# Kernel optimization log

Hardware: AMD Instinct MI355X
Metric: run time of the kernel (lower is better)

## Reference

```python
import jax, jax.numpy as jnp
import numpy as np
from jax import lax

N_INPUTS = 8
N_OUTPUTS = 4
N_RESERVOIR = 2048
T = 4096
SPECTRAL_RADIUS = 0.95
NOISE = 0.001


def setup_inputs() -> dict:
    key = jax.random.key(0)
    ks = jax.random.split(key, 8)
    inputs = jax.random.normal(ks[0], (T, N_INPUTS), dtype=jnp.float32)
    outputs = jax.random.normal(ks[1], (T, N_OUTPUTS), dtype=jnp.float32)
    # recurrent weights: uniform(-0.5, 0.5), rescaled to spectral radius ~0.95.
    # For a uniform(-0.5,0.5) NxN matrix the spectral radius is ~ sqrt(N/12)
    # (circular law), used here in place of an explicit eigendecomposition.
    w_raw = jax.random.uniform(ks[2], (N_RESERVOIR, N_RESERVOIR), dtype=jnp.float32) - 0.5
    radius = jnp.sqrt(N_RESERVOIR / 12.0)
    w = w_raw * (SPECTRAL_RADIUS / radius)
    w_in = jax.random.uniform(ks[3], (N_RESERVOIR, N_INPUTS), dtype=jnp.float32) * 2.0 - 1.0
    w_feedb = jax.random.uniform(ks[4], (N_RESERVOIR, N_OUTPUTS), dtype=jnp.float32) * 2.0 - 1.0
    # readout (nn.Linear): weight [n_out, R+n_in], bias [n_out]
    fan_in = N_RESERVOIR + N_INPUTS
    bound = 1.0 / np.sqrt(fan_in)
    lin_w = jax.random.uniform(ks[5], (N_OUTPUTS, fan_in), dtype=jnp.float32, minval=-bound, maxval=bound)
    lin_b = jax.random.uniform(ks[6], (N_OUTPUTS,), dtype=jnp.float32, minval=-bound, maxval=bound)
    # per-step regularization noise: noise * (uniform - 0.5), pre-drawn for determinism
    noise_seq = NOISE * (jax.random.uniform(ks[7], (T, N_RESERVOIR), dtype=jnp.float32) - 0.5)
    return {"inputs": inputs, "outputs": outputs, "w": w, "w_in": w_in,
            "w_feedb": w_feedb, "lin_w": lin_w, "lin_b": lin_b, "noise_seq": noise_seq}


def reference(inputs, outputs, w, w_in, w_feedb, lin_w, lin_b, noise_seq):
    # Echo-state recurrence: x_n = tanh(w @ x_{n-1} + w_in @ u_n + w_feedb @ y_{n-1}) + noise_n
    # States row 0 stays zero (original loop starts at n=1).
    R = w.shape[0]

    def step(x, per_step):
        u_n, y_prev, nz = per_step
        x_new = jnp.tanh(w @ x + w_in @ u_n + w_feedb @ y_prev) + nz
        return x_new, x_new

    x0 = jnp.zeros((R,), dtype=inputs.dtype)
    _, xs = lax.scan(step, x0, (inputs[1:], outputs[:-1], noise_seq[1:]))  # [T-1, R]

    zero_row_x = jnp.zeros((1, R), dtype=inputs.dtype)
    zero_row_u = jnp.zeros((1, inputs.shape[1]), dtype=inputs.dtype)
    states_x = jnp.concatenate([zero_row_x, xs], axis=0)              # [T, R]
    states_u = jnp.concatenate([zero_row_u, inputs[1:]], axis=0)       # [T, n_in]
    states = jnp.concatenate([states_x, states_u], axis=1)             # [T, R+n_in]

    out = states @ lin_w.T + lin_b                                     # [T, n_out]
    return out
```

## Files before the change

kernel.cpp:

```cpp
#include <hip/hip_runtime.h>

#define T_STEPS 4096
#define RSIZE   2048
#define N_IN    8
#define N_OUT   4
#define NWG     256
#define NT      256
#define LIN_STRIDE  (RSIZE + N_IN)
#define SENTINEL    0x7FC00000u

typedef float v4 __attribute__((ext_vector_type(4)));


__global__ __launch_bounds__(256) void init_kernel(v4* __restrict__ states4) {
    int idx = blockIdx.x * 256 + threadIdx.x;
    const float s = __uint_as_float(SENTINEL);
    v4 v = (idx < RSIZE / 4) ? (v4){0.f, 0.f, 0.f, 0.f} : (v4){s, s, s, s};
    states4[idx] = v;
}

__device__ __forceinline__ float dot4(v4 a, v4 b) {
    float s = a.x * b.x;
    s = fmaf(a.y, b.y, s);
    s = fmaf(a.z, b.z, s);
    s = fmaf(a.w, b.w, s);
    return s;
}

__global__ __launch_bounds__(NT, 1) void reservoir_kernel(
    const float* __restrict__ W,
    const float* __restrict__ Win,
    const float* __restrict__ Wfb,
    const float* __restrict__ inputs,
    const float* __restrict__ outputs,
    const float* __restrict__ noise,
    float* __restrict__ states)
{
    const int g    = blockIdx.x;
    const int t    = threadIdx.x;
    const int lane = t & 63;
    const int wv   = t >> 6;
    const int wid  = g * 4 + wv;
    const int r0   = wid * 2;

    v4 wreg[2][8];
    #pragma unroll
    for (int i = 0; i < 2; ++i)
        #pragma unroll
        for (int c = 0; c < 8; ++c)
            wreg[i][c] = *(const v4*)(W + (size_t)(r0 + i) * RSIZE + c * 256 + lane * 4);

    float win[N_IN] = {0}, wfb[N_OUT] = {0};
    if (lane < 2) {
        const int r = r0 + lane;
        #pragma unroll
        for (int j = 0; j < N_IN; ++j)  win[j] = Win[r * N_IN + j];
        #pragma unroll
        for (int k = 0; k < N_OUT; ++k) wfb[k] = Wfb[r * N_OUT + k];
    }

    __shared__ v4 xsh[2][RSIZE / 4];
    const int fi0 = wv * 128 + lane;
    const int fi1 = wv * 128 + 64 + lane;

    float cur_pre = 0.0f, cur_nz = 0.0f;
    if (lane < 2) {
        const int r = r0 + lane;
        cur_nz = noise[(size_t)RSIZE + r];
        v4 i0 = *(const v4*)(inputs + N_IN);
        v4 i1 = *(const v4*)(inputs + N_IN + 4);
        v4 o0 = *(const v4*)(outputs);
        float p = 0.0f;
        p = fmaf(win[0], i0.x, p); p = fmaf(win[1], i0.y, p);
        p = fmaf(win[2], i0.z, p); p = fmaf(win[3], i0.w, p);
        p = fmaf(win[4], i1.x, p); p = fmaf(win[5], i1.y, p);
        p = fmaf(win[6], i1.z, p); p = fmaf(win[7], i1.w, p);
        p = fmaf(wfb[0], o0.x, p); p = fmaf(wfb[1], o0.y, p);
        p = fmaf(wfb[2], o0.z, p); p = fmaf(wfb[3], o0.w, p);
        cur_pre = p;
    }

    for (int n = 1; n < T_STEPS; ++n) {
        const bool hn = (n + 1 < T_STEPS);
        v4 ni0 = {0.f,0.f,0.f,0.f}, ni1 = {0.f,0.f,0.f,0.f}, no0 = {0.f,0.f,0.f,0.f};
        float nnz = 0.0f;
        if (lane < 2 && hn) {
            ni0 = *(const v4*)(inputs + (size_t)(n + 1) * N_IN);
            ni1 = *(const v4*)(inputs + (size_t)(n + 1) * N_IN + 4);
            no0 = *(const v4*)(outputs + (size_t)n * N_OUT);
            nnz = noise[(size_t)(n + 1) * RSIZE + r0 + lane];
        }

        const volatile v4* base =
            (const volatile v4*)(states + (size_t)(n - 1) * RSIZE);
        v4 a = {0.f, 0.f, 0.f, 0.f}, b = {0.f, 0.f, 0.f, 0.f};
        bool done = false;
        for (;;) {
            if (!done) {
                a = base[fi0];
                b = base[fi1];
                done = (__float_as_uint(a.x) != SENTINEL) &
                       (__float_as_uint(a.y) != SENTINEL) &
                       (__float_as_uint(a.z) != SENTINEL) &
                       (__float_as_uint(a.w) != SENTINEL) &
                       (__float_as_uint(b.x) != SENTINEL) &
                       (__float_as_uint(b.y) != SENTINEL) &
                       (__float_as_uint(b.z) != SENTINEL) &
                       (__float_as_uint(b.w) != SENTINEL);
            }
            if (__all(done)) break;
            __builtin_amdgcn_s_sleep(1);
        }

        const int p = (n - 1) & 1;
        xsh[p][fi0] = a;
        xsh[p][fi1] = b;
        __syncthreads();

        float a0 = 0.f, a1 = 0.f, b0 = 0.f, b1 = 0.f;
        #pragma unroll
        for (int c = 0; c < 4; ++c) {
            v4 x0 = xsh[p][c * 64 + lane];
            v4 x1 = xsh[p][(c + 4) * 64 + lane];
            a0 += dot4(wreg[0][c], x0);
            b0 += dot4(wreg[0][c + 4], x1);
            a1 += dot4(wreg[1][c], x0);
            b1 += dot4(wreg[1][c + 4], x1);
        }
        float acc0 = a0 + b0;
        float acc1 = a1 + b1;

        float mine  = (lane & 1) ? acc1 : acc0;
        float other = (lane & 1) ? acc0 : acc1;
        mine += __shfl_xor(other, 1, 64);
        mine += __shfl_xor(mine, 2, 64);
        mine += __shfl_xor(mine, 4, 64);
        mine += __shfl_xor(mine, 8, 64);
        mine += __shfl_xor(mine, 16, 64);
        mine += __shfl_xor(mine, 32, 64);

        if (lane < 2) {
            float xn = tanhf(mine + cur_pre) + cur_nz;
            *(volatile float*)(states + (size_t)n * RSIZE + r0 + lane) = xn;
        }

        if (lane < 2 && hn) {
            float pnext = 0.0f;
            pnext = fmaf(win[0], ni0.x, pnext); pnext = fmaf(win[1], ni0.y, pnext);
            pnext = fmaf(win[2], ni0.z, pnext); pnext = fmaf(win[3], ni0.w, pnext);
            pnext = fmaf(win[4], ni1.x, pnext); pnext = fmaf(win[5], ni1.y, pnext);
            pnext = fmaf(win[6], ni1.z, pnext); pnext = fmaf(win[7], ni1.w, pnext);
            pnext = fmaf(wfb[0], no0.x, pnext); pnext = fmaf(wfb[1], no0.y, pnext);
            pnext = fmaf(wfb[2], no0.z, pnext); pnext = fmaf(wfb[3], no0.w, pnext);
            cur_pre = pnext;
            cur_nz  = nnz;
        }
    }
}

__global__ __launch_bounds__(256) void readout_kernel(
    const float* __restrict__ states,
    const float* __restrict__ inputs,
    const float* __restrict__ lin_w,
    const float* __restrict__ lin_b,
    float* __restrict__ out)
{
    const int ti   = blockIdx.x;
    const int tid  = threadIdx.x;
    const int lane = tid & 63;
    const int wave = tid >> 6;
    const int c0   = tid * 8;

    const float* xp = states + (size_t)ti * RSIZE + c0;
    v4 xa = *(const v4*)xp;
    v4 xb = *(const v4*)(xp + 4);

    float acc[N_OUT];
    #pragma unroll
    for (int o = 0; o < N_OUT; ++o) {
        const float* lp = lin_w + (size_t)o * LIN_STRIDE + c0;
        v4 la = *(const v4*)lp;
        v4 lb = *(const v4*)(lp + 4);
        acc[o] = dot4(la, xa) + dot4(lb, xb);
    }

    #pragma unroll
    for (int m = 1; m < 64; m <<= 1) {
        #pragma unroll
        for (int o = 0; o < N_OUT; ++o) acc[o] += __shfl_xor(acc[o], m, 64);
    }

    __shared__ float red[4][N_OUT];
    if (lane == 0) {
        #pragma unroll
        for (int o = 0; o < N_OUT; ++o) red[wave][o] = acc[o];
    }
    __syncthreads();

    if (tid < N_OUT) {
        float s = red[0][tid] + red[1][tid] + red[2][tid] + red[3][tid] + lin_b[tid];
        if (ti > 0) {
            #pragma unroll
            for (int j = 0; j < N_IN; ++j)
                s = fmaf(lin_w[(size_t)tid * LIN_STRIDE + RSIZE + j],
                         inputs[ti * N_IN + j], s);
        }
        out[ti * N_OUT + tid] = s;
    }
}

extern "C" void kernel_launch(void* const* d_in, const int* in_sizes, int n_in,
                              void* d_out, int out_size, void* d_ws, size_t ws_size,
                              hipStream_t stream) {
    const float* inputs  = (const float*)d_in[0];
    const float* outputs = (const float*)d_in[1];
    const float* W       = (const float*)d_in[2];
    const float* Win     = (const float*)d_in[3];
    const float* Wfb     = (const float*)d_in[4];
    const float* lin_w   = (const float*)d_in[5];
    const float* lin_b   = (const float*)d_in[6];
    const float* noise   = (const float*)d_in[7];
    float* out = (float*)d_out;

    float* states = (float*)d_ws;

    hipLaunchKernelGGL(init_kernel, dim3((T_STEPS * RSIZE / 4) / 256), dim3(256), 0,
                       stream, (v4*)states);
    hipLaunchKernelGGL(reservoir_kernel, dim3(NWG), dim3(NT), 0, stream,
                       W, Win, Wfb, inputs, outputs, noise, states);
    hipLaunchKernelGGL(readout_kernel, dim3(T_STEPS), dim3(256), 0, stream,
                       states, inputs, lin_w, lin_b, out);
}
```

Before: 8.104 ms.

## Have each wave poll full state vector directly, dropping LDS staging and block barrier

Each wave now reads the whole previous state vector from global memory and polls every element for the sentinel itself. This removes the shared-memory staging copy and the __syncthreads that coupled the four waves of a workgroup. The cost is four times as many global/L2 loads per step, with each wave spinning on all 2048 entries. Per-step input loads are made volatile and an explicit waitcnt is added after the state store.

```diff
diff --git a/kernel.cpp b/kernel.cpp
--- a/kernel.cpp
+++ b/kernel.cpp
@@ -25,6 +25,13 @@
     s = fmaf(a.z, b.z, s);
     s = fmaf(a.w, b.w, s);
     return s;
+}
+
+__device__ __forceinline__ bool ok4(v4 a) {
+    return (__float_as_uint(a.x) != SENTINEL) &
+           (__float_as_uint(a.y) != SENTINEL) &
+           (__float_as_uint(a.z) != SENTINEL) &
+           (__float_as_uint(a.w) != SENTINEL);
 }
 
 __global__ __launch_bounds__(NT, 1) void reservoir_kernel(
@@ -59,10 +66,6 @@
         for (int k = 0; k < N_OUT; ++k) wfb[k] = Wfb[r * N_OUT + k];
     }
 
-    __shared__ v4 xsh[2][RSIZE / 4];
-    const int fi0 = wv * 128 + lane;
-    const int fi1 = wv * 128 + 64 + lane;
-
     float cur_pre = 0.0f, cur_nz = 0.0f;
     if (lane < 2) {
         const int r = r0 + lane;
@@ -85,48 +88,42 @@
         v4 ni0 = {0.f,0.f,0.f,0.f}, ni1 = {0.f,0.f,0.f,0.f}, no0 = {0.f,0.f,0.f,0.f};
         float nnz = 0.0f;
         if (lane < 2 && hn) {
-            ni0 = *(const v4*)(inputs + (size_t)(n + 1) * N_IN);
-            ni1 = *(const v4*)(inputs + (size_t)(n + 1) * N_IN + 4);
-            no0 = *(const v4*)(outputs + (size_t)n * N_OUT);
-            nnz = noise[(size_t)(n + 1) * RSIZE + r0 + lane];
+            ni0 = *(const volatile v4*)(inputs + (size_t)(n + 1) * N_IN);
+            ni1 = *(const volatile v4*)(inputs + (size_t)(n + 1) * N_IN + 4);
+            no0 = *(const volatile v4*)(outputs + (size_t)n * N_OUT);
+            nnz = *(const volatile float*)(noise + (size_t)(n + 1) * RSIZE + r0 + lane);
         }
 
         const volatile v4* base =
             (const volatile v4*)(states + (size_t)(n - 1) * RSIZE);
-        v4 a = {0.f, 0.f, 0.f, 0.f}, b = {0.f, 0.f, 0.f, 0.f};
+        v4 x0, x1, x2, x3, x4, x5, x6, x7;
         bool done = false;
         for (;;) {
             if (!done) {
-                a = base[fi0];
-                b = base[fi1];
-                done = (__float_as_uint(a.x) != SENTINEL) &
-                       (__float_as_uint(a.y) != SENTINEL) &
-                       (__float_as_uint(a.z) != SENTINEL) &
-                       (__float_as_uint(a.w) != SENTINEL) &
-                       (__float_as_uint(b.x) != SENTINEL) &
-                       (__float_as_uint(b.y) != SENTINEL) &
-                       (__float_as_uint(b.z) != SENTINEL) &
-                       (__float_as_uint(b.w) != SENTINEL);
+                x0 = base[0 * 64 + lane];
+                x1 = base[1 * 64 + lane];
+                x2 = base[2 * 64 + lane];
+                x3 = base[3 * 64 + lane];
+                x4 = base[4 * 64 + lane];
+                x5 = base[5 * 64 + lane];
+                x6 = base[6 * 64 + lane];
+                x7 = base[7 * 64 + lane];
+                done = ok4(x0) & ok4(x1) & ok4(x2) & ok4(x3) &
+                       ok4(x4) & ok4(x5) & ok4(x6) & ok4(x7);
             }
             if (__all(done)) break;
             __builtin_amdgcn_s_sleep(1);
         }
 
-        const int p = (n - 1) & 1;
-        xsh[p][fi0] = a;
-        xsh[p][fi1] = b;
-        __syncthreads();
-
-        float a0 = 0.f, a1 = 0.f, b0 = 0.f, b1 = 0.f;
-        #pragma unroll
-        for (int c = 0; c < 4; ++c) {
-            v4 x0 = xsh[p][c * 64 + lane];
-            v4 x1 = xsh[p][(c + 4) * 64 + lane];
-            a0 += dot4(wreg[0][c], x0);
-            b0 += dot4(wreg[0][c + 4], x1);
-            a1 += dot4(wreg[1][c], x0);
-            b1 += dot4(wreg[1][c + 4], x1);
-        }
+        float a0, a1, b0, b1;
+        a0  = dot4(wreg[0][0], x0); a1  = dot4(wreg[1][0], x0);
+        b0  = dot4(wreg[0][4], x4); b1  = dot4(wreg[1][4], x4);
+        a0 += dot4(wreg[0][1], x1); a1 += dot4(wreg[1][1], x1);
+        b0 += dot4(wreg[0][5], x5); b1 += dot4(wreg[1][5], x5);
+        a0 += dot4(wreg[0][2], x2); a1 += dot4(wreg[1][2], x2);
+        b0 += dot4(wreg[0][6], x6); b1 += dot4(wreg[1][6], x6);
+        a0 += dot4(wreg[0][3], x3); a1 += dot4(wreg[1][3], x3);
+        b0 += dot4(wreg[0][7], x7); b1 += dot4(wreg[1][7], x7);
         float acc0 = a0 + b0;
         float acc1 = a1 + b1;
 
@@ -143,6 +140,7 @@
             float xn = tanhf(mine + cur_pre) + cur_nz;
             *(volatile float*)(states + (size_t)n * RSIZE + r0 + lane) = xn;
         }
+        __builtin_amdgcn_s_waitcnt(0);
 
         if (lane < 2 && hn) {
             float pnext = 0.0f;
```

Result: slower. 16.45 ms (+103.0%).
